# Kernel tuning notes

Hardware: AMD Instinct MI355X
Metric: run time of the kernel (lower is better)

The kernel has to match this reference:

```python
import jax, jax.numpy as jnp
import numpy as np

# --- dims ---
B_, H_IMG, W_IMG = 8, 64, 1024
C1, C2 = 32, 64
DM = 1024          # token channels = C2 * H_IMG/4
DI = 2048          # d_inner = expand * d_model
DS = 64            # d_state
DC = 4             # d_conv
NH, HD = 32, 64    # n_heads, headdim
DCONV_DIM = DI + 2 * DS           # 2176 (ngroups=1)
DPROJ = 2 * DI + 2 * DS + NH      # 4256
NB = 4             # num mamba blocks
FFH = 2 * DM       # feed-forward hidden
EPS = 1e-5


def bn(x, p, axis=1):
    # eval-mode batchnorm; p = [gamma, beta, running_mean, running_var] stacked [4, C]
    sh = [1] * x.ndim
    sh[axis] = -1
    g, b, m, v = (p[i].reshape(sh) for i in range(4))
    return (x - m) * jax.lax.rsqrt(v + EPS) * g + b


def conv2d(x, w, stride, pad):
    return jax.lax.conv_general_dilated(
        x, w, (stride, stride), [(pad, pad), (pad, pad)],
        dimension_numbers=("NCHW", "OIHW", "NCHW"))


def mamba2(u, Wi, cw, cb, dtb, A_log, Dp, nw, Wo):
    # u: [B, L, DM]  (faithful Mamba2 forward: in_proj -> causal depthwise conv
    #  + silu -> selective state scan -> gated RMSNorm -> out_proj)
    Bsz, L, _ = u.shape
    zxbcdt = jnp.einsum('bld,pd->blp', u, Wi)                  # [B,L,DPROJ]
    z, xBC, dt = jnp.split(zxbcdt, [DI, DI + DCONV_DIM], axis=-1)
    dt = jax.nn.softplus(dt + dtb)                             # [B,L,NH]
    xp = jnp.pad(xBC, ((0, 0), (DC - 1, 0), (0, 0)))           # causal pad
    xBC = sum(xp[:, k:k + L, :] * cw[:, k] for k in range(DC)) + cb
    xBC = jax.nn.silu(xBC)
    x, Bm, Cm = jnp.split(xBC, [DI, DI + DS], axis=-1)         # x:[B,L,DI] B/C:[B,L,DS]
    x = x.reshape(Bsz, L, NH, HD)
    A = -jnp.exp(A_log)                                        # [NH]
    dA = jnp.exp(dt * A)                                       # [B,L,NH]
    dtx = dt[..., None] * x                                    # [B,L,NH,HD]

    def step(h, inp):
        dA_t, dtx_t, B_t, C_t = inp
        h = h * dA_t[..., None, None] + dtx_t[..., None] * B_t[:, None, None, :]
        return h, jnp.einsum('bhpn,bn->bhp', h, C_t)

    h0 = jnp.zeros((Bsz, NH, HD, DS), u.dtype)
    _, ys = jax.lax.scan(step, h0, (dA.transpose(1, 0, 2),
                                    dtx.transpose(1, 0, 2, 3),
                                    Bm.transpose(1, 0, 2),
                                    Cm.transpose(1, 0, 2)))
    y = ys.transpose(1, 0, 2, 3) + Dp[None, None, :, None] * x  # D skip
    y = y.reshape(Bsz, L, DI)
    y = y * jax.nn.silu(z)                                      # gate
    y = y * jax.lax.rsqrt(jnp.mean(y * y, -1, keepdims=True) + EPS) * nw
    return jnp.einsum('bld,od->blo', y, Wo)                     # [B,L,DM]


def setup_inputs() -> dict:
    key = jax.random.key(0)
    ks = iter(jax.random.split(key, 80))

    def nrm(shape, s=0.02):
        return jax.random.normal(next(ks), shape, jnp.float32) * s

    def bnp(c):
        return jnp.stack([jax.random.uniform(next(ks), (c,), minval=0.5, maxval=1.5),
                          nrm((c,), 0.1), nrm((c,), 0.1),
                          jax.random.uniform(next(ks), (c,), minval=0.5, maxval=1.5)])

    inp = dict(
        image=jax.random.normal(next(ks), (B_, 1, H_IMG, W_IMG), jnp.float32),
        conv1_w=nrm((C1, 1, 7, 7), 0.1), bn1=bnp(C1),
        conv2_w=nrm((C2, C1, 7, 7), 0.05), bn2=bnp(C2),
        ds_w=nrm((C2, 1, 1, 1), 0.1), ds_bn=bnp(C2),
        in_proj_w=nrm((NB, DPROJ, DM)),
        conv1d_w=nrm((NB, DCONV_DIM, DC), 0.2), conv1d_b=nrm((NB, DCONV_DIM), 0.1),
        dt_bias=jnp.log(jnp.expm1(jax.random.uniform(next(ks), (NB, NH), minval=0.001, maxval=0.1))),
        A_log=jnp.log(jax.random.uniform(next(ks), (NB, NH), minval=1.0, maxval=16.0)),
        D=jax.random.uniform(next(ks), (NB, NH)),
        norm_w=jnp.ones((NB, DI), jnp.float32),
        out_proj_w=nrm((NB, DM, DI)),
        blk_bn=jnp.stack([bnp(DM) for _ in range(NB)]),
        ff_w1=nrm((NB, FFH, DM)), ff_b1=nrm((NB, FFH), 0.1),
        ff_bn1=jnp.stack([bnp(FFH) for _ in range(NB)]),
        ff_w2=nrm((NB, DM, FFH)), ff_b2=nrm((NB, DM), 0.1),
        ff_bn2=jnp.stack([bnp(DM) for _ in range(NB)]),
    )
    return inp


def reference(image, conv1_w, bn1, conv2_w, bn2, ds_w, ds_bn,
              in_proj_w, conv1d_w, conv1d_b, dt_bias, A_log, D, norm_w,
              out_proj_w, blk_bn, ff_w1, ff_b1, ff_bn1, ff_w2, ff_b2, ff_bn2):
    # --- conv stem with residual downsample ---
    x = bn(conv2d(image, conv1_w, 2, 3), bn1)
    x = bn(conv2d(x, conv2_w, 2, 3), bn2)
    res = bn(conv2d(image, ds_w, 4, 0), ds_bn)
    x = jax.nn.relu(x + res)                       # [B,C2,H/4,W/4]
    tokens = x.reshape(x.shape[0], -1, x.shape[3])  # image_to_sequence -> [B,DM,L]

    for i in range(NB):
        # SSMBlock: mamba2 + BN + residual
        residual = tokens
        t = mamba2(tokens.transpose(0, 2, 1), in_proj_w[i], conv1d_w[i],
                   conv1d_b[i], dt_bias[i], A_log[i], D[i], norm_w[i],
                   out_proj_w[i]).transpose(0, 2, 1)
        tokens = bn(t, blk_bn[i]) + residual
        # FeedForward (1x1 conv MLP) with residual
        residual = tokens
        h = jax.nn.relu(bn(jnp.einsum('oc,bcl->bol', ff_w1[i], tokens)
                           + ff_b1[i][:, None], ff_bn1[i]))
        tokens = bn(jnp.einsum('oc,bcl->bol', ff_w2[i], h)
                    + ff_b2[i][:, None], ff_bn2[i]) + residual
    return tokens  # [B, DM, L]
```

## Files before the change

kernel.cpp:

```cpp
#include <hip/hip_runtime.h>
#include <hip/hip_bf16.h>
#include <hip/hip_fp16.h>
#include <math.h>

#define EPSF 1e-5f
#define B_N 8
#define L_N 256
#define DM_N 1024
#define DI_N 2048
#define DS_N 64
#define NH_N 32
#define HD_N 64
#define DCONV_N 2176
#define DPROJ_N 4256
#define NTOK 2048
#define FFH_N 2048
#define NPAD_INPROJ 4352

typedef _Float16 f16x8 __attribute__((ext_vector_type(8)));
typedef float f32x4 __attribute__((ext_vector_type(4)));

__device__ __forceinline__ float sigf(float x) { return 1.f / (1.f + __expf(-x)); }

__device__ __forceinline__ void gll16(const void* g, void* l) {
  typedef __attribute__((address_space(1))) const void gv;
  typedef __attribute__((address_space(3))) void lv;
  __builtin_amdgcn_global_load_lds((gv*)g, (lv*)l, 16, 0, 0);
}

__device__ __forceinline__ f16x8 cvt8(float4 a, float4 b) {
  f16x8 o;
  o[0] = (_Float16)a.x; o[1] = (_Float16)a.y; o[2] = (_Float16)a.z; o[3] = (_Float16)a.w;
  o[4] = (_Float16)b.x; o[5] = (_Float16)b.y; o[6] = (_Float16)b.z; o[7] = (_Float16)b.w;
  return o;
}

__global__ __launch_bounds__(256) void k_tohalf8(
    const float* __restrict__ src, _Float16* __restrict__ dst, int n, int ntot) {
  int i = (blockIdx.x * 256 + threadIdx.x) * 8;
  if (i >= ntot) return;
  f16x8 o;
  if (i < n) {
    float4 a = *(const float4*)(src + i);
    float4 b = *(const float4*)(src + i + 4);
    o = cvt8(a, b);
  } else {
#pragma unroll
    for (int j = 0; j < 8; ++j) o[j] = (_Float16)0.f;
  }
  *(f16x8*)(dst + i) = o;
}

__global__ __launch_bounds__(256) void k_w1t(
    const float* __restrict__ w1, _Float16* __restrict__ W1t) {
  int i = blockIdx.x * 256 + threadIdx.x;
  if (i >= 32 * 64) return;
  int co = i >> 6, k = i & 63;
  W1t[i] = (k < 49) ? (_Float16)w1[co * 49 + k] : (_Float16)0.f;
}

__global__ __launch_bounds__(256) void k_conv1m(
    const float* __restrict__ img, const _Float16* __restrict__ W1t,
    const float* __restrict__ bnp, _Float16* __restrict__ X1h) {
  __shared__ float sIn[7][264];
  __shared__ _Float16 sA[128][72];
  __shared__ _Float16 sB[32][72];
  int b = blockIdx.x, y = blockIdx.y, x0 = blockIdx.z * 128;
  int t = threadIdx.x;
  {
    int r = t >> 3, c = (t & 7) * 8;
    *(f16x8*)&sB[r][c] = *(const f16x8*)&W1t[r * 64 + c];
  }
  const float* ip = img + (size_t)b * 64 * 1024;
#pragma unroll
  for (int r = 0; r < 7; ++r) {
    int yy = 2 * y - 3 + r;
    for (int c = t; c < 262; c += 256) {
      int xx = 2 * x0 - 3 + c;
      float v = 0.f;
      if (yy >= 0 && yy < 64 && xx >= 0 && xx < 1024) v = ip[yy * 1024 + xx];
      sIn[r][c] = v;
    }
  }
  __syncthreads();
  {
    int p = t >> 1, half = t & 1;
    _Float16 av[32];
    if (half == 0) {
#pragma unroll
      for (int k = 0; k < 32; ++k)
        av[k] = (_Float16)sIn[k / 7][2 * p + (k % 7)];
    } else {
#pragma unroll
      for (int k = 32; k < 64; ++k)
        av[k - 32] = (k < 49) ? (_Float16)sIn[k / 7][2 * p + (k % 7)] : (_Float16)0.f;
    }
    *(f16x8*)&sA[p][half * 32 + 0] = *(f16x8*)&av[0];
    *(f16x8*)&sA[p][half * 32 + 8] = *(f16x8*)&av[8];
    *(f16x8*)&sA[p][half * 32 + 16] = *(f16x8*)&av[16];
    *(f16x8*)&sA[p][half * 32 + 24] = *(f16x8*)&av[24];
  }
  __syncthreads();
  int w = t >> 6, lane = t & 63, lr = lane & 15, kh = lane >> 4;
  f32x4 acc[2][2];
#pragma unroll
  for (int i = 0; i < 2; ++i)
#pragma unroll
    for (int j = 0; j < 2; ++j) acc[i][j] = (f32x4)(0.f);
#pragma unroll
  for (int ks = 0; ks < 2; ++ks) {
    f16x8 af[2], bf[2];
#pragma unroll
    for (int i = 0; i < 2; ++i)
      af[i] = *(const f16x8*)&sA[w * 32 + i * 16 + lr][ks * 32 + kh * 8];
#pragma unroll
    for (int j = 0; j < 2; ++j)
      bf[j] = *(const f16x8*)&sB[j * 16 + lr][ks * 32 + kh * 8];
#pragma unroll
    for (int i = 0; i < 2; ++i)
#pragma unroll
      for (int j = 0; j < 2; ++j)
        acc[i][j] = __builtin_amdgcn_mfma_f32_16x16x32_f16(af[i], bf[j], acc[i][j], 0, 0, 0);
  }
#pragma unroll
  for (int j = 0; j < 2; ++j) {
    int co = j * 16 + lr;
    float g = bnp[co], be = bnp[32 + co], mm = bnp[64 + co], vv = bnp[96 + co];
    float sc = rsqrtf(vv + EPSF) * g, sh = be - mm * sc;
#pragma unroll
    for (int i = 0; i < 2; ++i) {
#pragma unroll
      for (int rr = 0; rr < 4; ++rr) {
        int pix = w * 32 + i * 16 + kh * 4 + rr;
        int x = x0 + pix;
        X1h[((size_t)(b * 32 + y) * 512 + x) * 32 + co] =
            (_Float16)fmaf(acc[i][j][rr], sc, sh);
      }
    }
  }
}

__global__ __launch_bounds__(256) void k_w2t(
    const float* __restrict__ w2, _Float16* __restrict__ W2t) {
  int i = blockIdx.x * 256 + threadIdx.x;
  if (i >= 49 * 64 * 32) return;
  int ci = i & 31, co = (i >> 5) & 63, rs = i >> 11;
  W2t[rs * 2048 + co * 32 + ci] = (_Float16)w2[co * 1568 + ci * 49 + rs];
}

__global__ __launch_bounds__(256) void k_conv2m(
    const _Float16* __restrict__ X1h, const _Float16* __restrict__ W2t,
    const float* __restrict__ bn2p, const float* __restrict__ img,
    const float* __restrict__ dsw, const float* __restrict__ dsbnp,
    _Float16* __restrict__ Tok16) {
  __shared__ _Float16 As[2][64 * 72];
  __shared__ _Float16 Bs[2][64 * 72];
  int b = blockIdx.x, ho = blockIdx.y, wo0 = blockIdx.z * 64;
  int t = threadIdx.x;
  int w = t >> 6, lane = t & 63;
  int lr = lane & 15, kh = lane >> 4;
  int wm = w >> 1, wn = w & 1;
  f32x4 acc[2][2];
#pragma unroll
  for (int i = 0; i < 2; ++i)
#pragma unroll
    for (int j = 0; j < 2; ++j) acc[i][j] = (f32x4)(0.f);

  const _Float16* xb = X1h + (size_t)b * 32 * 512 * 32;

  auto LOADA = [&](int step, int u, f16x8& ra) {
    int c = u * 256 + t;
    int row = c >> 3, s = c & 7;
    int rsl = s >> 2, ciq = s & 3;
    int rs = step * 2 + rsl;
#pragma unroll
    for (int q = 0; q < 8; ++q) ra[q] = (_Float16)0.f;
    if (rs < 49) {
      int r = rs / 7, ss = rs - 7 * r;
      int y = 2 * ho + r - 3, xx = 2 * (wo0 + row) + ss - 3;
      if (y >= 0 && y < 32 && xx >= 0 && xx < 512)
        ra = *(const f16x8*)(xb + ((size_t)(y * 512 + xx)) * 32 + ciq * 8);
    }
  };
  auto LOADB = [&](int step, int u, f16x8& rb) {
    int c = u * 256 + t;
    int co = c >> 3, s = c & 7;
    int rsl = s >> 2, ciq = s & 3;
    int rs = step * 2 + rsl;
#pragma unroll
    for (int q = 0; q < 8; ++q) rb[q] = (_Float16)0.f;
    if (rs < 49) rb = *(const f16x8*)(W2t + rs * 2048 + co * 32 + ciq * 8);
  };

  f16x8 ra[2], rb[2];
#pragma unroll
  for (int u = 0; u < 2; ++u) { LOADA(0, u, ra[u]); LOADB(0, u, rb[u]); }
#pragma unroll
  for (int u = 0; u < 2; ++u) {
    int c = u * 256 + t, row = c >> 3, s = c & 7;
    *(f16x8*)&As[0][row * 72 + s * 8] = ra[u];
    *(f16x8*)&Bs[0][row * 72 + s * 8] = rb[u];
  }
  __syncthreads();

  int cur = 0;
  for (int st = 0; st < 25; ++st) {
    f16x8 na[2], nb[2];
    if (st + 1 < 25) {
#pragma unroll
      for (int u = 0; u < 2; ++u) { LOADA(st + 1, u, na[u]); LOADB(st + 1, u, nb[u]); }
    }
    f16x8 af[2][2], bf[2][2];
#pragma unroll
    for (int i = 0; i < 2; ++i)
#pragma unroll
      for (int kk = 0; kk < 2; ++kk)
        af[i][kk] = *(const f16x8*)&As[cur][(wm * 32 + i * 16 + lr) * 72 + (kk * 4 + kh) * 8];
#pragma unroll
    for (int j = 0; j < 2; ++j)
#pragma unroll
      for (int kk = 0; kk < 2; ++kk)
        bf[j][kk] = *(const f16x8*)&Bs[cur][(wn * 32 + j * 16 + lr) * 72 + (kk * 4 + kh) * 8];
#pragma unroll
    for (int kk = 0; kk < 2; ++kk)
#pragma unroll
      for (int i = 0; i < 2; ++i)
#pragma unroll
        for (int j = 0; j < 2; ++j)
          acc[i][j] = __builtin_amdgcn_mfma_f32_16x16x32_f16(af[i][kk], bf[j][kk], acc[i][j], 0, 0, 0);
    if (st + 1 < 25) {
#pragma unroll
      for (int u = 0; u < 2; ++u) {
        int c = u * 256 + t, row = c >> 3, s = c & 7;
        *(f16x8*)&As[cur ^ 1][row * 72 + s * 8] = na[u];
        *(f16x8*)&Bs[cur ^ 1][row * 72 + s * 8] = nb[u];
      }
      __syncthreads();
      cur ^= 1;
    }
  }

#pragma unroll
  for (int j = 0; j < 2; ++j) {
    int co = wn * 32 + j * 16 + lr;
    float g = bn2p[co], be = bn2p[64 + co], mm = bn2p[128 + co], vv = bn2p[192 + co];
    float sc = rsqrtf(vv + EPSF) * g, sh = be - mm * sc;
    float dg = dsbnp[co], dbe = dsbnp[64 + co], dmm = dsbnp[128 + co], dvv = dsbnp[192 + co];
    float dsc = rsqrtf(dvv + EPSF) * dg, dsh = dbe - dmm * dsc;
    float wv = dsw[co];
#pragma unroll
    for (int i = 0; i < 2; ++i) {
#pragma unroll
      for (int rr = 0; rr < 4; ++rr) {
        int row = wm * 32 + i * 16 + kh * 4 + rr;
        int wo = wo0 + row;
        float dval = fmaf(img[((size_t)(b * 64 + 4 * ho)) * 1024 + 4 * wo] * wv, dsc, dsh);
        float v = fmaf(acc[i][j][rr], sc, sh) + dval;
        v = v > 0.f ? v : 0.f;
        Tok16[((size_t)(b * 256 + wo)) * DM_N + co * 16 + ho] = (_Float16)v;
      }
    }
  }
}

template <int MODE, int BM, int BN>
__global__ __launch_bounds__(256) void k_mgemm(
    const _Float16* __restrict__ A, const _Float16* __restrict__ W,
    int M, int N, int K,
    const float* __restrict__ bias, const float* __restrict__ bnp,
    const _Float16* __restrict__ res16, _Float16* __restrict__ C16) {
  constexpr int MI = BM / 32, NJ = BN / 32;
  __shared__ _Float16 As[2][BM * 64];
  __shared__ _Float16 Bs[2][BN * 64];
  const int t = threadIdx.x;
  const int w = t >> 6, lane = t & 63;
  const int lr = lane & 15, kh = lane >> 4;
  const int wm = w >> 1, wn = w & 1;
  const int m0 = blockIdx.y * BM, n0 = blockIdx.x * BN;
  f32x4 acc[MI][NJ];
#pragma unroll
  for (int i = 0; i < MI; ++i)
#pragma unroll
    for (int j = 0; j < NJ; ++j) acc[i][j] = (f32x4)(0.f);

  const int nt = K >> 6;
  auto STAGE = [&](int bb, int kt) {
    const int k0 = kt << 6;
#pragma unroll
    for (int it = 0; it < BM / 32; ++it) {
      int c = it * 256 + w * 64 + lane;
      int row = c >> 3, s = c & 7;
      int kg = (s ^ (row & 7)) * 8;
      gll16(A + (size_t)(m0 + row) * K + k0 + kg,
            &As[bb][(size_t)(it * 256 + w * 64) * 8]);
    }
#pragma unroll
    for (int it = 0; it < BN / 32; ++it) {
      int c = it * 256 + w * 64 + lane;
      int row = c >> 3, s = c & 7;
      int kg = (s ^ (row & 7)) * 8;
      gll16(W + (size_t)(n0 + row) * K + k0 + kg,
            &Bs[bb][(size_t)(it * 256 + w * 64) * 8]);
    }
  };

  STAGE(0, 0);
  __syncthreads();
  int bb = 0;
  const int sw = lr & 7;
  for (int kt = 0; kt < nt; ++kt) {
    if (kt + 1 < nt) STAGE(bb ^ 1, kt + 1);
    f16x8 af[MI][2], bf[NJ][2];
#pragma unroll
    for (int i = 0; i < MI; ++i)
#pragma unroll
      for (int kk = 0; kk < 2; ++kk)
        af[i][kk] = *(const f16x8*)&As[bb][(size_t)(wm * (BM / 2) + i * 16 + lr) * 64 +
                                           ((kk * 4 + kh) ^ sw) * 8];
#pragma unroll
    for (int j = 0; j < NJ; ++j)
#pragma unroll
      for (int kk = 0; kk < 2; ++kk)
        bf[j][kk] = *(const f16x8*)&Bs[bb][(size_t)(wn * (BN / 2) + j * 16 + lr) * 64 +
                                           ((kk * 4 + kh) ^ sw) * 8];
#pragma unroll
    for (int kk = 0; kk < 2; ++kk)
#pragma unroll
      for (int i = 0; i < MI; ++i)
#pragma unroll
        for (int j = 0; j < NJ; ++j)
          acc[i][j] = __builtin_amdgcn_mfma_f32_16x16x32_f16(af[i][kk], bf[j][kk], acc[i][j], 0, 0, 0);
    __syncthreads();
    bb ^= 1;
  }

#pragma unroll
  for (int j = 0; j < NJ; ++j) {
    int cn = n0 + wn * (BN / 2) + j * 16 + lr;
    if (cn >= N) continue;
    float sc = 1.f, sh = 0.f, bs = 0.f;
    if (MODE >= 1) {
      float g = bnp[cn], be = bnp[N + cn];
      float mm = bnp[2 * N + cn], vv = bnp[3 * N + cn];
      sc = rsqrtf(vv + EPSF) * g;
      sh = be - mm * sc;
    }
    if (MODE == 2 || MODE == 3) bs = bias[cn];
#pragma unroll
    for (int i = 0; i < MI; ++i) {
#pragma unroll
      for (int rr = 0; rr < 4; ++rr) {
        int r = m0 + wm * (BM / 2) + i * 16 + kh * 4 + rr;
        float v = acc[i][j][rr];
        if (MODE == 2 || MODE == 3) v += bs;
        if (MODE >= 1) v = fmaf(v, sc, sh);
        if (MODE == 2) v = v > 0.f ? v : 0.f;
        size_t o = (size_t)r * N + cn;
        if (MODE == 1 || MODE == 3) v += (float)res16[o];
        C16[o] = (_Float16)v;
      }
    }
  }
}

__global__ __launch_bounds__(256) void k_convprep(
    const _Float16* __restrict__ ZX16, const float* __restrict__ cw,
    const float* __restrict__ cb, const float* __restrict__ dtb,
    const float* __restrict__ Alog, _Float16* __restrict__ XBC16,
    float* __restrict__ DT, float* __restrict__ DLA) {
  int m = blockIdx.x;
  int c = blockIdx.y * 256 + threadIdx.x;
  int l = m & 255;
  if (c < DCONV_N) {
    const float* cwp = cw + c * 4;
    float acc = cb[c];
#pragma unroll
    for (int k = 0; k < 4; ++k) {
      int dl = l + k - 3;
      if (dl >= 0)
        acc = fmaf((float)ZX16[(size_t)(m + k - 3) * DPROJ_N + DI_N + c], cwp[k], acc);
    }
    XBC16[(size_t)m * DCONV_N + c] = (_Float16)(acc * sigf(acc));
  } else if (c < DCONV_N + NH_N) {
    int h = c - DCONV_N;
    float xx = (float)ZX16[(size_t)m * DPROJ_N + DI_N + DCONV_N + h] + dtb[h];
    float dt = xx > 20.f ? xx : log1pf(__expf(xx));
    DT[m * NH_N + h] = dt;
    DLA[m * NH_N + h] = -dt * __expf(Alog[h]);
  }
}

__global__ __launch_bounds__(256) void k_scan(
    const _Float16* __restrict__ XBC16, const float* __restrict__ DT,
    const float* __restrict__ DLA, const float* __restrict__ Dp,
    float* __restrict__ Y) {
  __shared__ _Float16 sC[64][72];
  __shared__ _Float16 sB[64][72];
  __shared__ _Float16 sBts[64][72];
  __shared__ _Float16 sXt[64][72];
  __shared__ _Float16 sP[64][72];
  __shared__ _Float16 sH[64][72];
  __shared__ float sH32[64][68];
  __shared__ float sS[64], sEl[64], sEs[64], sDt[64];
  __shared__ float sCpt;

  const int b = blockIdx.x >> 5, h = blockIdx.x & 31;
  const int t = threadIdx.x;
  const int w = t >> 6, lane = t & 63;
  const int lr = lane & 15, kh = lane >> 4;
  const float Dh = Dp[h];

  {
    _Float16* hp = &sH[0][0];
    float* h32p = &sH32[0][0];
    for (int i = t; i < 64 * 72; i += 256) hp[i] = (_Float16)0.f;
    for (int i = t; i < 64 * 68; i += 256) h32p[i] = 0.f;
  }

  for (int c = 0; c < 4; ++c) {
    const int mbase = b * L_N + c * 64;
    __syncthreads();

    if (t < 64) {
      int l = t;
      float v = DLA[(mbase + l) * NH_N + h];
#pragma unroll
      for (int o = 1; o < 64; o <<= 1) {
        float u = __shfl_up(v, o);
        v += (l >= o) ? u : 0.f;
      }
      sS[l] = v;
      sEl[l] = __expf(v);
      float s63 = __shfl(v, 63);
      sEs[l] = __expf(s63 - v);
      if (l == 63) sCpt = __expf(s63);
      sDt[l] = DT[(mbase + l) * NH_N + h];
    }
    __syncthreads();

    {
      int l = t >> 2, q = t & 3;
      const _Float16* row = XBC16 + (size_t)(mbase + l) * DCONV_N;
      float dt_l = sDt[l], es_l = sEs[l];
      f16x8 b0 = *(const f16x8*)&row[DI_N + q * 16];
      f16x8 b1 = *(const f16x8*)&row[DI_N + q * 16 + 8];
      *(f16x8*)&sB[l][q * 16] = b0;
      *(f16x8*)&sB[l][q * 16 + 8] = b1;
#pragma unroll
      for (int i = 0; i < 8; ++i) {
        sBts[q * 16 + i][l] = (_Float16)((float)b0[i] * es_l);
        sBts[q * 16 + 8 + i][l] = (_Float16)((float)b1[i] * es_l);
      }
      *(f16x8*)&sC[l][q * 16] = *(const f16x8*)&row[DI_N + DS_N + q * 16];
      *(f16x8*)&sC[l][q * 16 + 8] = *(const f16x8*)&row[DI_N + DS_N + q * 16 + 8];
      f16x8 x0 = *(const f16x8*)&row[h * HD_N + q * 16];
      f16x8 x1 = *(const f16x8*)&row[h * HD_N + q * 16 + 8];
#pragma unroll
      for (int i = 0; i < 8; ++i) {
        sXt[q * 16 + i][l] = (_Float16)((float)x0[i] * dt_l);
        sXt[q * 16 + 8 + i][l] = (_Float16)((float)x1[i] * dt_l);
      }
    }
    __syncthreads();

    f32x4 Sacc[4], Yacc[4];
#pragma unroll
    for (int j = 0; j < 4; ++j) { Sacc[j] = (f32x4)(0.f); Yacc[j] = (f32x4)(0.f); }
    {
      f16x8 aC[2];
#pragma unroll
      for (int kk = 0; kk < 2; ++kk)
        aC[kk] = *(const f16x8*)&sC[16 * w + lr][kk * 32 + kh * 8];
#pragma unroll
      for (int kk = 0; kk < 2; ++kk)
#pragma unroll
        for (int jt = 0; jt < 4; ++jt) {
          f16x8 bB = *(const f16x8*)&sB[jt * 16 + lr][kk * 32 + kh * 8];
          f16x8 bH = *(const f16x8*)&sH[jt * 16 + lr][kk * 32 + kh * 8];
          Sacc[jt] = __builtin_amdgcn_mfma_f32_16x16x32_f16(aC[kk], bB, Sacc[jt], 0, 0, 0);
          Yacc[jt] = __builtin_amdgcn_mfma_f32_16x16x32_f16(aC[kk], bH, Yacc[jt], 0, 0, 0);
        }
    }

#pragma unroll
    for (int rr = 0; rr < 4; ++rr) {
      int l = 16 * w + kh * 4 + rr;
      float sl = sS[l], el = sEl[l];
#pragma unroll
      for (int jt = 0; jt < 4; ++jt) {
        int j = jt * 16 + lr;
        float pv = (j <= l) ? Sacc[jt][rr] * __expf(sl - sS[j]) : 0.f;
        sP[l][j] = (_Float16)pv;
        Yacc[jt][rr] *= el;
      }
    }
    __syncthreads();

    f32x4 Hacc[4];
#pragma unroll
    for (int j = 0; j < 4; ++j) Hacc[j] = (f32x4)(0.f);
    {
      f16x8 aP[2], aX[2];
#pragma unroll
      for (int kk = 0; kk < 2; ++kk) {
        aP[kk] = *(const f16x8*)&sP[16 * w + lr][kk * 32 + kh * 8];
        aX[kk] = *(const f16x8*)&sXt[16 * w + lr][kk * 32 + kh * 8];
      }
#pragma unroll
      for (int kk = 0; kk < 2; ++kk)
#pragma unroll
        for (int jt = 0; jt < 4; ++jt) {
          f16x8 bX = *(const f16x8*)&sXt[jt * 16 + lr][kk * 32 + kh * 8];
          f16x8 bBt = *(const f16x8*)&sBts[jt * 16 + lr][kk * 32 + kh * 8];
          Yacc[jt] = __builtin_amdgcn_mfma_f32_16x16x32_f16(aP[kk], bX, Yacc[jt], 0, 0, 0);
          Hacc[jt] = __builtin_amdgcn_mfma_f32_16x16x32_f16(aX[kk], bBt, Hacc[jt], 0, 0, 0);
        }
    }

    float cpt = sCpt;
#pragma unroll
    for (int rr = 0; rr < 4; ++rr) {
      int lrow = 16 * w + kh * 4 + rr;
      int m = mbase + lrow;
#pragma unroll
      for (int jt = 0; jt < 4; ++jt) {
        int p = jt * 16 + lr;
        float xr = (float)XBC16[(size_t)m * DCONV_N + h * HD_N + p];
        Y[(size_t)m * DI_N + h * HD_N + p] = fmaf(Dh, xr, Yacc[jt][rr]);
        float hv = fmaf(cpt, sH32[lrow][jt * 16 + lr], Hacc[jt][rr]);
        sH32[lrow][jt * 16 + lr] = hv;
        sH[lrow][jt * 16 + lr] = (_Float16)hv;
      }
    }
  }
}

__global__ __launch_bounds__(256) void k_gatenorm(
    const float* __restrict__ Y, const _Float16* __restrict__ ZX16,
    const float* __restrict__ nw, _Float16* __restrict__ YN16) {
  int m = blockIdx.x, t = threadIdx.x;
  const float* y = Y + (size_t)m * DI_N;
  const _Float16* z = ZX16 + (size_t)m * DPROJ_N;
  int c0 = t * 8;
  float4 y0 = *(const float4*)&y[c0];
  float4 y1 = *(const float4*)&y[c0 + 4];
  f16x8 z8 = *(const f16x8*)&z[c0];
  float yv[8] = {y0.x, y0.y, y0.z, y0.w, y1.x, y1.y, y1.z, y1.w};
  float vals[8];
  float ss = 0.f;
#pragma unroll
  for (int j = 0; j < 8; ++j) {
    float zz = (float)z8[j];
    float vv = yv[j] * zz * sigf(zz);
    vals[j] = vv;
    ss = fmaf(vv, vv, ss);
  }
#pragma unroll
  for (int o = 1; o < 64; o <<= 1) ss += __shfl_xor(ss, o);
  __shared__ float sred[4];
  if ((t & 63) == 0) sred[t >> 6] = ss;
  __syncthreads();
  float tot = sred[0] + sred[1] + sred[2] + sred[3];
  float scale = rsqrtf(tot * (1.f / DI_N) + EPSF);
  float4 nw0 = *(const float4*)&nw[c0];
  float4 nw1 = *(const float4*)&nw[c0 + 4];
  float nv[8] = {nw0.x, nw0.y, nw0.z, nw0.w, nw1.x, nw1.y, nw1.z, nw1.w};
  f16x8 o;
#pragma unroll
  for (int j = 0; j < 8; ++j) o[j] = (_Float16)(vals[j] * scale * nv[j]);
  *(f16x8*)&YN16[(size_t)m * DI_N + c0] = o;
}

__global__ __launch_bounds__(256) void k_transpose(
    const _Float16* __restrict__ Tok16, float* __restrict__ out) {
  __shared__ float tile[32][33];
  int d0 = blockIdx.x * 32, m0 = blockIdx.y * 32;
  int tx = threadIdx.x & 31, ty = threadIdx.x >> 5;
  for (int i = ty; i < 32; i += 8)
    tile[i][tx] = (float)Tok16[(size_t)(m0 + i) * DM_N + d0 + tx];
  __syncthreads();
  int b = m0 >> 8, l0 = m0 & 255;
  for (int i = ty; i < 32; i += 8)
    out[((size_t)b * DM_N + d0 + i) * L_N + l0 + tx] = tile[tx][i];
}

extern "C" void kernel_launch(void* const* d_in, const int* in_sizes, int n_in,
                              void* d_out, int out_size, void* d_ws, size_t ws_size,
                              hipStream_t stream) {
  const float* image = (const float*)d_in[0];
  const float* conv1_w = (const float*)d_in[1];
  const float* bn1 = (const float*)d_in[2];
  const float* conv2_w = (const float*)d_in[3];
  const float* bn2 = (const float*)d_in[4];
  const float* ds_w = (const float*)d_in[5];
  const float* ds_bn = (const float*)d_in[6];
  const float* in_proj_w = (const float*)d_in[7];
  const float* conv1d_w = (const float*)d_in[8];
  const float* conv1d_b = (const float*)d_in[9];
  const float* dt_bias = (const float*)d_in[10];
  const float* A_log = (const float*)d_in[11];
  const float* Dpar = (const float*)d_in[12];
  const float* norm_w = (const float*)d_in[13];
  const float* out_proj_w = (const float*)d_in[14];
  const float* blk_bn = (const float*)d_in[15];
  const float* ff_w1 = (const float*)d_in[16];
  const float* ff_b1 = (const float*)d_in[17];
  const float* ff_bn1 = (const float*)d_in[18];
  const float* ff_w2 = (const float*)d_in[19];
  const float* ff_b2 = (const float*)d_in[20];
  const float* ff_bn2 = (const float*)d_in[21];

  float* ws = (float*)d_ws;
  float* YR = ws;
  float* DTb = YR + (size_t)NTOK * DI_N;
  float* DLAb = DTb + (size_t)NTOK * NH_N;
  _Float16* Tok16 = (_Float16*)(DLAb + (size_t)NTOK * NH_N);
  _Float16* ZX16 = Tok16 + (size_t)NTOK * DM_N;
  _Float16* XBC16 = ZX16 + (size_t)NTOK * DPROJ_N;
  _Float16* YN16 = XBC16 + (size_t)NTOK * DCONV_N;
  _Float16* H116 = YN16 + (size_t)NTOK * DI_N;
  _Float16* W16 = H116 + (size_t)NTOK * DI_N;
  _Float16* W2t = W16 + (size_t)NPAD_INPROJ * DM_N;
  _Float16* W1t = W2t + (size_t)49 * 64 * 32;
  _Float16* X1h = (_Float16*)YR;

  k_w1t<<<8, 256, 0, stream>>>(conv1_w, W1t);
  k_conv1m<<<dim3(8, 32, 4), 256, 0, stream>>>(image, W1t, bn1, X1h);
  k_w2t<<<(49 * 64 * 32 + 255) / 256, 256, 0, stream>>>(conv2_w, W2t);
  k_conv2m<<<dim3(8, 16, 4), 256, 0, stream>>>(X1h, W2t, bn2, image, ds_w, ds_bn, Tok16);

  for (int i = 0; i < 4; ++i) {
    const float* Wi = in_proj_w + (size_t)i * DPROJ_N * DM_N;
    const float* cw = conv1d_w + (size_t)i * DCONV_N * 4;
    const float* cb = conv1d_b + (size_t)i * DCONV_N;
    const float* dtb = dt_bias + i * NH_N;
    const float* al = A_log + i * NH_N;
    const float* dd = Dpar + i * NH_N;
    const float* nw = norm_w + i * DI_N;
    const float* Wo = out_proj_w + (size_t)i * DM_N * DI_N;
    const float* bbn = blk_bn + (size_t)i * 4 * DM_N;
    const float* w1 = ff_w1 + (size_t)i * FFH_N * DM_N;
    const float* b1 = ff_b1 + i * FFH_N;
    const float* fbn1 = ff_bn1 + (size_t)i * 4 * FFH_N;
    const float* w2 = ff_w2 + (size_t)i * DM_N * FFH_N;
    const float* b2 = ff_b2 + i * DM_N;
    const float* fbn2 = ff_bn2 + (size_t)i * 4 * DM_N;

    k_tohalf8<<<(NPAD_INPROJ * 1024 / 8 + 255) / 256, 256, 0, stream>>>(
        Wi, W16, DPROJ_N * DM_N, NPAD_INPROJ * DM_N);
    k_mgemm<0, 64, 128><<<dim3(34, 32), 256, 0, stream>>>(
        Tok16, W16, NTOK, DPROJ_N, DM_N, nullptr, nullptr, nullptr, ZX16);
    k_convprep<<<dim3(NTOK, 9), 256, 0, stream>>>(ZX16, cw, cb, dtb, al, XBC16, DTb, DLAb);
    k_scan<<<256, 256, 0, stream>>>(XBC16, DTb, DLAb, dd, YR);
    k_gatenorm<<<NTOK, 256, 0, stream>>>(YR, ZX16, nw, YN16);
    k_tohalf8<<<(DM_N * DI_N / 8 + 255) / 256, 256, 0, stream>>>(
        Wo, W16, DM_N * DI_N, DM_N * DI_N);
    k_mgemm<1, 64, 64><<<dim3(16, 32), 256, 0, stream>>>(
        YN16, W16, NTOK, DM_N, DI_N, nullptr, bbn, Tok16, Tok16);
    k_tohalf8<<<(FFH_N * DM_N / 8 + 255) / 256, 256, 0, stream>>>(
        w1, W16, FFH_N * DM_N, FFH_N * DM_N);
    k_mgemm<2, 64, 128><<<dim3(16, 32), 256, 0, stream>>>(
        Tok16, W16, NTOK, FFH_N, DM_N, b1, fbn1, nullptr, H116);
    k_tohalf8<<<(DM_N * FFH_N / 8 + 255) / 256, 256, 0, stream>>>(
        w2, W16, DM_N * FFH_N, DM_N * FFH_N);
    k_mgemm<3, 64, 64><<<dim3(16, 32), 256, 0, stream>>>(
        H116, W16, NTOK, DM_N, FFH_N, b2, fbn2, Tok16, Tok16);
  }
  k_transpose<<<dim3(32, 64), 256, 0, stream>>>(Tok16, (float*)d_out);
}
```

Baseline: 691.4 us.

## Fuse fp32-to-fp16 weight conversion into GEMM staging and enlarge in_proj tile

Removes the separate weight-conversion kernels and their fp16 workspace round trip. The GEMM now reads fp32 weights directly, converts them to fp16 in registers, and writes them to shared memory, with zero-fill past N. The in_proj GEMM also moves to a 128x128 tile. In exchange, weight tiles go through synchronous register loads instead of async global-to-LDS copies, each weight tile is reconverted by every M-block, and global weight traffic doubles in bytes.

```diff
diff --git a/kernel.cpp b/kernel.cpp
--- a/kernel.cpp
+++ b/kernel.cpp
@@ -15,7 +15,6 @@
 #define DPROJ_N 4256
 #define NTOK 2048
 #define FFH_N 2048
-#define NPAD_INPROJ 4352
 
 typedef _Float16 f16x8 __attribute__((ext_vector_type(8)));
 typedef float f32x4 __attribute__((ext_vector_type(4)));
@@ -33,22 +32,6 @@
   o[0] = (_Float16)a.x; o[1] = (_Float16)a.y; o[2] = (_Float16)a.z; o[3] = (_Float16)a.w;
   o[4] = (_Float16)b.x; o[5] = (_Float16)b.y; o[6] = (_Float16)b.z; o[7] = (_Float16)b.w;
   return o;
-}
-
-__global__ __launch_bounds__(256) void k_tohalf8(
-    const float* __restrict__ src, _Float16* __restrict__ dst, int n, int ntot) {
-  int i = (blockIdx.x * 256 + threadIdx.x) * 8;
-  if (i >= ntot) return;
-  f16x8 o;
-  if (i < n) {
-    float4 a = *(const float4*)(src + i);
-    float4 b = *(const float4*)(src + i + 4);
-    o = cvt8(a, b);
-  } else {
-#pragma unroll
-    for (int j = 0; j < 8; ++j) o[j] = (_Float16)0.f;
-  }
-  *(f16x8*)(dst + i) = o;
 }
 
 __global__ __launch_bounds__(256) void k_w1t(
@@ -265,7 +248,7 @@
 
 template <int MODE, int BM, int BN>
 __global__ __launch_bounds__(256) void k_mgemm(
-    const _Float16* __restrict__ A, const _Float16* __restrict__ W,
+    const _Float16* __restrict__ A, const float* __restrict__ W32,
     int M, int N, int K,
     const float* __restrict__ bias, const float* __restrict__ bnp,
     const _Float16* __restrict__ res16, _Float16* __restrict__ C16) {
@@ -288,19 +271,28 @@
     const int k0 = kt << 6;
 #pragma unroll
     for (int it = 0; it < BM / 32; ++it) {
-      int c = it * 256 + w * 64 + lane;
+      int c = it * 256 + t;
       int row = c >> 3, s = c & 7;
       int kg = (s ^ (row & 7)) * 8;
-      gll16(A + (size_t)(m0 + row) * K + k0 + kg,
-            &As[bb][(size_t)(it * 256 + w * 64) * 8]);
+      gll16(A + (size_t)(m0 + row) * K + k0 + kg, &As[bb][(size_t)c * 8]);
     }
 #pragma unroll
     for (int it = 0; it < BN / 32; ++it) {
-      int c = it * 256 + w * 64 + lane;
+      int c = it * 256 + t;
       int row = c >> 3, s = c & 7;
       int kg = (s ^ (row & 7)) * 8;
-      gll16(W + (size_t)(n0 + row) * K + k0 + kg,
-            &Bs[bb][(size_t)(it * 256 + w * 64) * 8]);
+      int rn = n0 + row;
+      f16x8 v;
+      if (rn < N) {
+        const float* wp = W32 + (size_t)rn * K + k0 + kg;
+        float4 a = *(const float4*)wp;
+        float4 b = *(const float4*)(wp + 4);
+        v = cvt8(a, b);
+      } else {
+#pragma unroll
+        for (int q = 0; q < 8; ++q) v[q] = (_Float16)0.f;
+      }
+      *(f16x8*)&Bs[bb][(size_t)c * 8] = v;
     }
   };
 
@@ -619,8 +611,7 @@
   _Float16* XBC16 = ZX16 + (size_t)NTOK * DPROJ_N;
   _Float16* YN16 = XBC16 + (size_t)NTOK * DCONV_N;
   _Float16* H116 = YN16 + (size_t)NTOK * DI_N;
-  _Float16* W16 = H116 + (size_t)NTOK * DI_N;
-  _Float16* W2t = W16 + (size_t)NPAD_INPROJ * DM_N;
+  _Float16* W2t = H116 + (size_t)NTOK * DI_N;
   _Float16* W1t = W2t + (size_t)49 * 64 * 32;
   _Float16* X1h = (_Float16*)YR;
 
@@ -646,25 +637,17 @@
     const float* b2 = ff_b2 + i * DM_N;
     const float* fbn2 = ff_bn2 + (size_t)i * 4 * DM_N;
 
-    k_tohalf8<<<(NPAD_INPROJ * 1024 / 8 + 255) / 256, 256, 0, stream>>>(
-        Wi, W16, DPROJ_N * DM_N, NPAD_INPROJ * DM_N);
-    k_mgemm<0, 64, 128><<<dim3(34, 32), 256, 0, stream>>>(
-        Tok16, W16, NTOK, DPROJ_N, DM_N, nullptr, nullptr, nullptr, ZX16);
+    k_mgemm<0, 128, 128><<<dim3(34, 16), 256, 0, stream>>>(
+        Tok16, Wi, NTOK, DPROJ_N, DM_N, nullptr, nullptr, nullptr, ZX16);
     k_convprep<<<dim3(NTOK, 9), 256, 0, stream>>>(ZX16, cw, cb, dtb, al, XBC16, DTb, DLAb);
     k_scan<<<256, 256, 0, stream>>>(XBC16, DTb, DLAb, dd, YR);
     k_gatenorm<<<NTOK, 256, 0, stream>>>(YR, ZX16, nw, YN16);
-    k_tohalf8<<<(DM_N * DI_N / 8 + 255) / 256, 256, 0, stream>>>(
-        Wo, W16, DM_N * DI_N, DM_N * DI_N);
     k_mgemm<1, 64, 64><<<dim3(16, 32), 256, 0, stream>>>(
-        YN16, W16, NTOK, DM_N, DI_N, nullptr, bbn, Tok16, Tok16);
-    k_tohalf8<<<(FFH_N * DM_N / 8 + 255) / 256, 256, 0, stream>>>(
-        w1, W16, FFH_N * DM_N, FFH_N * DM_N);
+        YN16, Wo, NTOK, DM_N, DI_N, nullptr, bbn, Tok16, Tok16);
     k_mgemm<2, 64, 128><<<dim3(16, 32), 256, 0, stream>>>(
-        Tok16, W16, NTOK, FFH_N, DM_N, b1, fbn1, nullptr, H116);
-    k_tohalf8<<<(DM_N * FFH_N / 8 + 255) / 256, 256, 0, stream>>>(
-        w2, W16, DM_N * FFH_N, DM_N * FFH_N);
+        Tok16, w1, NTOK, FFH_N, DM_N, b1, fbn1, nullptr, H116);
     k_mgemm<3, 64, 64><<<dim3(16, 32), 256, 0, stream>>>(
-        H116, W16, NTOK, DM_N, FFH_N, b2, fbn2, Tok16, Tok16);
+        H116, w2, NTOK, DM_N, FFH_N, b2, fbn2, Tok16, Tok16);
   }
   k_transpose<<<dim3(32, 64), 256, 0, stream>>>(Tok16, (float*)d_out);
 }
```

Result: slower. 962.5 us (+39.2%).
